# Kernel optimization log

Hardware: AMD Instinct MI355X
Metric: run time of the kernel (lower is better)

## Reference

```python
import jax, jax.numpy as jnp
import numpy as np

N_NODES = 100000
HIDDEN = 128
N_CLASS = 10
N_EDGES = 1600000


def setup_inputs() -> dict:
    key = jax.random.key(0)
    ks = jax.random.split(key, 8)
    s = 1.0 / np.sqrt(HIDDEN)
    return {
        "edge_index": jax.random.randint(ks[0], (2, N_EDGES), 0, N_NODES, dtype=jnp.int32),
        "embedding": jax.random.normal(ks[1], (N_NODES, HIDDEN), jnp.float32),
        "W1": jax.random.normal(ks[2], (HIDDEN, HIDDEN), jnp.float32) * s,
        "b1": jnp.zeros((HIDDEN,), jnp.float32),
        "W2": jax.random.normal(ks[3], (HIDDEN, HIDDEN), jnp.float32) * s,
        "b2": jnp.zeros((HIDDEN,), jnp.float32),
        "W_out": jax.random.normal(ks[4], (HIDDEN, N_CLASS), jnp.float32) * s,
        "b_out": jnp.zeros((N_CLASS,), jnp.float32),
    }


def reference(edge_index, embedding, W1, b1, W2, b2, W_out, b_out):
    N = embedding.shape[0]
    # PyG GCNConv: add self-loops, symmetric normalization D^-1/2 (A+I) D^-1/2
    loops = jnp.arange(N, dtype=edge_index.dtype)
    src = jnp.concatenate([edge_index[0], loops])  # message sources
    dst = jnp.concatenate([edge_index[1], loops])  # aggregation targets
    deg = jax.ops.segment_sum(jnp.ones_like(dst, jnp.float32), dst, num_segments=N)
    inv_sqrt = jnp.where(deg > 0, jax.lax.rsqrt(jnp.maximum(deg, 1.0)), 0.0)
    norm = inv_sqrt[src] * inv_sqrt[dst]  # [E+N]

    x = embedding  # forward ignores input x, uses learned embedding table
    for W, b in ((W1, b1), (W2, b2)):
        h = x @ W                                      # [N, H]
        msg = h[src] * norm[:, None]                   # gather + scale, [E+N, H]
        agg = jax.ops.segment_sum(msg, dst, num_segments=N)
        x = jax.nn.relu(agg + b)
    return x @ W_out + b_out
```

## Files before the change

kernel.cpp:

```cpp
#include <hip/hip_runtime.h>
#include <hip/hip_bf16.h>

#define HID 128
#define NCLASS 10
#define PCHUNK 8192
#define HB 256

typedef unsigned int uint;
typedef unsigned short ushort;
typedef __attribute__((ext_vector_type(8))) __bf16 bf16x8;
typedef __attribute__((ext_vector_type(4))) float f32x4;

__device__ __forceinline__ uint bf16rne(float x) {
    uint u = __float_as_uint(x);
    return (u + 0x7FFFu + ((u >> 16) & 1u)) >> 16;
}
__device__ __forceinline__ uint pack2(float e0, float e1) {
    return bf16rne(e0) | (bf16rne(e1) << 16);
}
__device__ __forceinline__ void unpack2(uint w, float& lo, float& hi) {
    lo = __uint_as_float(w << 16);
    hi = __uint_as_float(w & 0xFFFF0000u);
}
__device__ __forceinline__ void split2(float e0, float e1, uint& h, uint& l) {
    uint h0 = bf16rne(e0), h1 = bf16rne(e1);
    float r0 = e0 - __uint_as_float(h0 << 16);
    float r1 = e1 - __uint_as_float(h1 << 16);
    h = h0 | (h1 << 16);
    l = bf16rne(r0) | (bf16rne(r1) << 16);
}
__device__ __forceinline__ bf16x8 as_bf16x8(uint4 u) {
    return __builtin_bit_cast(bf16x8, u);
}
__device__ __forceinline__ void unpack8(uint4 u, float* f) {
    unpack2(u.x, f[0], f[1]); unpack2(u.y, f[2], f[3]);
    unpack2(u.z, f[4], f[5]); unpack2(u.w, f[6], f[7]);
}

__device__ __forceinline__ void pack_w_body(const float* __restrict__ W,
                                            uint* __restrict__ hi, uint* __restrict__ lo,
                                            int slot, int l) {
    const int s = slot >> 3, t = slot & 7;
    const int kb = s * 32 + (l >> 4) * 8, n = t * 16 + (l & 15);
    float f[8];
#pragma unroll
    for (int j = 0; j < 8; ++j) f[j] = W[(kb + j) * HID + n];
    uint4 h, lo4;
    split2(f[0], f[1], h.x, lo4.x);
    split2(f[2], f[3], h.y, lo4.y);
    split2(f[4], f[5], h.z, lo4.z);
    split2(f[6], f[7], h.w, lo4.w);
    const int fo = (slot * 64 + l) * 4;
    *(uint4*)(hi + fo) = h;
    *(uint4*)(lo + fo) = lo4;
}

__global__ __launch_bounds__(256) void hist_pack_kernel(
        const int* __restrict__ dst, int* __restrict__ bcnt, int E, int NB,
        const float* __restrict__ W1, uint* __restrict__ W1hi, uint* __restrict__ W1lo,
        const float* __restrict__ W2, uint* __restrict__ W2hi, uint* __restrict__ W2lo) {
    __shared__ int h[400];
    const int t = threadIdx.x;
    if ((int)blockIdx.x < HB) {
        const int ech = (E + HB - 1) / HB;
        const int e0 = blockIdx.x * ech;
        const int e1 = min(E, e0 + ech);
        for (int i = t; i < NB; i += 256) h[i] = 0;
        __syncthreads();
        for (int e = e0 + t; e < e1; e += 256) atomicAdd(&h[dst[e] >> 8], 1);
        __syncthreads();
        for (int i = t; i < NB; i += 256)
            if (h[i]) atomicAdd(&bcnt[i], h[i]);
    } else {
        const int pb = blockIdx.x - HB;
        const int slot = (pb & 7) * 4 + (t >> 6);
        const int l = t & 63;
        if (pb < 8) pack_w_body(W1, W1hi, W1lo, slot, l);
        else        pack_w_body(W2, W2hi, W2lo, slot, l);
    }
}

template <bool FP32IN>
__device__ __forceinline__ void gemm_body_mfma(
        const float* __restrict__ Xf, const uint* __restrict__ Xhi,
        const uint* __restrict__ Wphi, const uint* __restrict__ Wplo,
        ushort* __restrict__ HS, int N, int bidx, int tid) {
    const int wv = tid >> 6;
    const int l = tid & 63;
    const int q = l >> 4;
    const int cm = l & 15;
    const long rowbase = (long)bidx * 128 + wv * 32;

    bf16x8 bhi[2][4], blo[2][4];
#pragma unroll
    for (int rt = 0; rt < 2; ++rt) {
        const long row = rowbase + rt * 16 + cm;
        const long rc = row < N ? row : (N - 1);
#pragma unroll
        for (int s = 0; s < 4; ++s) {
            if (FP32IN) {
                const float* xp = Xf + rc * HID + s * 32 + q * 8;
                const float4 a0 = ((const float4*)xp)[0];
                const float4 a1 = ((const float4*)xp)[1];
                uint4 h, lo4;
                split2(a0.x, a0.y, h.x, lo4.x);
                split2(a0.z, a0.w, h.y, lo4.y);
                split2(a1.x, a1.y, h.z, lo4.z);
                split2(a1.z, a1.w, h.w, lo4.w);
                bhi[rt][s] = as_bf16x8(h);
                blo[rt][s] = as_bf16x8(lo4);
            } else {
                const long o = rc * (HID / 2) + s * 16 + q * 4;
                bhi[rt][s] = as_bf16x8(*(const uint4*)(Xhi + o));
            }
        }
    }

    f32x4 acc[2][8];
#pragma unroll
    for (int rt = 0; rt < 2; ++rt)
#pragma unroll
        for (int t = 0; t < 8; ++t) acc[rt][t] = (f32x4)0.0f;

#pragma unroll
    for (int s = 0; s < 4; ++s) {
#pragma unroll
        for (int t = 0; t < 8; ++t) {
            const int fo = ((s * 8 + t) * 64 + l) * 4;
            const bf16x8 whi = as_bf16x8(*(const uint4*)(Wphi + fo));
            const bf16x8 wlo = as_bf16x8(*(const uint4*)(Wplo + fo));
#pragma unroll
            for (int rt = 0; rt < 2; ++rt) {
                acc[rt][t] = __builtin_amdgcn_mfma_f32_16x16x32_bf16(whi, bhi[rt][s], acc[rt][t], 0, 0, 0);
                if (FP32IN)
                    acc[rt][t] = __builtin_amdgcn_mfma_f32_16x16x32_bf16(whi, blo[rt][s], acc[rt][t], 0, 0, 0);
                acc[rt][t] = __builtin_amdgcn_mfma_f32_16x16x32_bf16(wlo, bhi[rt][s], acc[rt][t], 0, 0, 0);
            }
        }
    }

#pragma unroll
    for (int rt = 0; rt < 2; ++rt) {
        const long row = rowbase + rt * 16 + cm;
        if (row < N) {
#pragma unroll
            for (int t = 0; t < 8; ++t) {
                uint2 o;
                o.x = pack2(acc[rt][t][0], acc[rt][t][1]);
                o.y = pack2(acc[rt][t][2], acc[rt][t][3]);
                *(uint2*)&HS[row * HID + t * 16 + q * 4] = o;
            }
        }
    }
}

__global__ __launch_bounds__(256) void gemm1_part_kernel(
        const float* __restrict__ emb, const uint* __restrict__ Wphi,
        const uint* __restrict__ Wplo, ushort* __restrict__ HS, int N,
        const int* __restrict__ src, const int* __restrict__ dst,
        int* __restrict__ gcursor, uint* __restrict__ staged, int E, int PB, int NB) {
    __shared__ int hist[400], lbase[400], loff[400];
    const int t = threadIdx.x;
    if ((int)blockIdx.x >= PB) {
        gemm_body_mfma<true>(emb, nullptr, Wphi, Wplo, HS, N, blockIdx.x - PB, t);
        return;
    }
    const int e0 = blockIdx.x * PCHUNK;
    for (int i = t; i < NB; i += 256) { hist[i] = 0; loff[i] = 0; }
    __syncthreads();
#pragma unroll
    for (int j = 0; j < PCHUNK / 256; ++j) {
        const int e = e0 + j * 256 + t;
        if (e < E) atomicAdd(&hist[dst[e] >> 8], 1);
    }
    __syncthreads();
    for (int b = t; b < NB; b += 256)
        if (hist[b] > 0) lbase[b] = atomicAdd(&gcursor[b], hist[b]);
    __syncthreads();
#pragma unroll
    for (int j = 0; j < PCHUNK / 256; ++j) {
        const int e = e0 + j * 256 + t;
        if (e < E) {
            const int d = dst[e];
            const int b = d >> 8;
            const int pos = lbase[b] + atomicAdd(&loff[b], 1);
            staged[pos] = (uint)src[e] | ((uint)(d & 255) << 17);
        }
    }
}

__global__ __launch_bounds__(256) void gemm2_kernel(
        const uint* __restrict__ Xhi, const uint* __restrict__ Wphi,
        const uint* __restrict__ Wplo, ushort* __restrict__ HS, int N) {
    gemm_body_mfma<false>(nullptr, Xhi, Wphi, Wplo, HS, N, blockIdx.x, threadIdx.x);
}

__global__ __launch_bounds__(512) void scan_buckets_kernel(const int* __restrict__ bcnt,
                                                           int* bbase, int* gcursor,
                                                           int* rps, int NB, int E, int N) {
    __shared__ int sh[512];
    const int t = threadIdx.x;
    const int v = (t < NB) ? bcnt[t] : 0;
    sh[t] = v;
    __syncthreads();
    for (int off = 1; off < 512; off <<= 1) {
        int x = (t >= off) ? sh[t - off] : 0;
        __syncthreads();
        sh[t] += x;
        __syncthreads();
    }
    const int excl = sh[t] - v;
    if (t < NB) { bbase[t] = excl; gcursor[t] = excl; }
    if (t == NB - 1) bbase[NB] = excl + v;
    if (t == 0) rps[N] = E;
}

__global__ __launch_bounds__(256) void fill_bucket_kernel(
        const uint* __restrict__ staged, const int* __restrict__ bbase,
        int* __restrict__ rps, float* __restrict__ invs, int* __restrict__ col, int N) {
    __shared__ int h[256], cur[256], sh[256];
    const int b = blockIdx.x, t = threadIdx.x;
    const int w0 = bbase[b], w1 = bbase[b + 1];
    const int base0 = b << 8;
    h[t] = 0;
    __syncthreads();
    for (int i = w0 + t; i < w1; i += 256) atomicAdd(&h[staged[i] >> 17], 1);
    __syncthreads();
    const int my = h[t];
    sh[t] = my;
    __syncthreads();
    for (int off = 1; off < 256; off <<= 1) {
        int x = (t >= off) ? sh[t - off] : 0;
        __syncthreads();
        sh[t] += x;
        __syncthreads();
    }
    const int start = w0 + sh[t] - my;
    cur[t] = start;
    const int node = base0 + t;
    if (node < N) {
        rps[node] = start;
        invs[node] = rsqrtf((float)my + 1.0f);
    }
    __syncthreads();
    for (int i = w0 + t; i < w1; i += 256) {
        const uint u = staged[i];
        const int p = atomicAdd(&cur[u >> 17], 1);
        col[p] = (int)(u & 0x1FFFFu);
    }
}

__global__ __launch_bounds__(256) void pull_relu_kernel(
        const int* __restrict__ rps, const int* __restrict__ col,
        const uint* __restrict__ HS, const float* __restrict__ invs,
        const float* __restrict__ b, uint* __restrict__ Xhi, int N) {
    const int g = blockIdx.x * 256 + threadIdx.x;
    const int node = g >> 3;
    if (node >= N) return;
    const int lane = g & 7;
    const int p = rps[node];
    const int d = rps[node + 1] - p;
    const uint4* H4 = (const uint4*)HS;
    const size_t so = (size_t)node * 16 + lane * 2;

    float acc[16];
    {
        const float sn = invs[node];
        float f[16];
        unpack8(H4[so], f);
        unpack8(H4[so + 1], f + 8);
#pragma unroll
        for (int j = 0; j < 16; ++j) acc[j] = f[j] * sn;
    }
    int i = 0;
    for (; i + 4 <= d; i += 4) {
        const int s0 = col[p + i], s1 = col[p + i + 1], s2 = col[p + i + 2], s3 = col[p + i + 3];
        const float w0 = invs[s0], w1 = invs[s1], w2 = invs[s2], w3 = invs[s3];
        const uint4 a0 = H4[(size_t)s0 * 16 + lane * 2], a0b = H4[(size_t)s0 * 16 + lane * 2 + 1];
        const uint4 a1 = H4[(size_t)s1 * 16 + lane * 2], a1b = H4[(size_t)s1 * 16 + lane * 2 + 1];
        const uint4 a2 = H4[(size_t)s2 * 16 + lane * 2], a2b = H4[(size_t)s2 * 16 + lane * 2 + 1];
        const uint4 a3 = H4[(size_t)s3 * 16 + lane * 2], a3b = H4[(size_t)s3 * 16 + lane * 2 + 1];
        float f[16];
        unpack8(a0, f); unpack8(a0b, f + 8);
#pragma unroll
        for (int j = 0; j < 16; ++j) acc[j] += f[j] * w0;
        unpack8(a1, f); unpack8(a1b, f + 8);
#pragma unroll
        for (int j = 0; j < 16; ++j) acc[j] += f[j] * w1;
        unpack8(a2, f); unpack8(a2b, f + 8);
#pragma unroll
        for (int j = 0; j < 16; ++j) acc[j] += f[j] * w2;
        unpack8(a3, f); unpack8(a3b, f + 8);
#pragma unroll
        for (int j = 0; j < 16; ++j) acc[j] += f[j] * w3;
    }
    for (; i < d; ++i) {
        const int s0 = col[p + i];
        const float w0 = invs[s0];
        const uint4 a0 = H4[(size_t)s0 * 16 + lane * 2], a0b = H4[(size_t)s0 * 16 + lane * 2 + 1];
        float f[16];
        unpack8(a0, f); unpack8(a0b, f + 8);
#pragma unroll
        for (int j = 0; j < 16; ++j) acc[j] += f[j] * w0;
    }
    const float sn = invs[node];
    float x[16];
#pragma unroll
    for (int j = 0; j < 16; ++j)
        x[j] = sn * fmaxf(acc[j] * sn + b[lane * 16 + j], 0.0f);
    uint4 h0, h1;
    h0.x = pack2(x[0], x[1]);   h0.y = pack2(x[2], x[3]);
    h0.z = pack2(x[4], x[5]);   h0.w = pack2(x[6], x[7]);
    h1.x = pack2(x[8], x[9]);   h1.y = pack2(x[10], x[11]);
    h1.z = pack2(x[12], x[13]); h1.w = pack2(x[14], x[15]);
    uint* oh = Xhi + (size_t)node * 64 + lane * 8;
    *(uint4*)oh = h0; *(uint4*)(oh + 4) = h1;
}

__global__ __launch_bounds__(256) void pull_out_kernel(
        const int* __restrict__ rps, const int* __restrict__ col,
        const uint* __restrict__ HS, const float* __restrict__ invs,
        const float* __restrict__ b2, const float* __restrict__ Wout,
        const float* __restrict__ bout, float* __restrict__ OUT, int N) {
    __shared__ float Wd[320 * 4];
    for (int t = threadIdx.x; t < 320; t += 256) {
        const int c = t >> 5, rem = t & 31, j4 = rem >> 3, l = rem & 7;
        const int k0 = l * 16 + j4 * 4;
        float4 w;
        w.x = Wout[(k0 + 0) * NCLASS + c];
        w.y = Wout[(k0 + 1) * NCLASS + c];
        w.z = Wout[(k0 + 2) * NCLASS + c];
        w.w = Wout[(k0 + 3) * NCLASS + c];
        ((float4*)Wd)[t] = w;
    }
    __syncthreads();

    const int g = blockIdx.x * 256 + threadIdx.x;
    const int node = g >> 3;
    if (node >= N) return;
    const int lane = g & 7;
    const int p = rps[node];
    const int d = rps[node + 1] - p;
    const uint4* H4 = (const uint4*)HS;
    const size_t so = (size_t)node * 16 + lane * 2;

    float acc[16];
    {
        float f[16];
        unpack8(H4[so], f);
        unpack8(H4[so + 1], f + 8);
#pragma unroll
        for (int j = 0; j < 16; ++j) acc[j] = f[j];
    }
    int i = 0;
    for (; i + 4 <= d; i += 4) {
        const int s0 = col[p + i], s1 = col[p + i + 1], s2 = col[p + i + 2], s3 = col[p + i + 3];
        const uint4 a0 = H4[(size_t)s0 * 16 + lane * 2], a0b = H4[(size_t)s0 * 16 + lane * 2 + 1];
        const uint4 a1 = H4[(size_t)s1 * 16 + lane * 2], a1b = H4[(size_t)s1 * 16 + lane * 2 + 1];
        const uint4 a2 = H4[(size_t)s2 * 16 + lane * 2], a2b = H4[(size_t)s2 * 16 + lane * 2 + 1];
        const uint4 a3 = H4[(size_t)s3 * 16 + lane * 2], a3b = H4[(size_t)s3 * 16 + lane * 2 + 1];
        float f[16];
        unpack8(a0, f); unpack8(a0b, f + 8);
#pragma unroll
        for (int j = 0; j < 16; ++j) acc[j] += f[j];
        unpack8(a1, f); unpack8(a1b, f + 8);
#pragma unroll
        for (int j = 0; j < 16; ++j) acc[j] += f[j];
        unpack8(a2, f); unpack8(a2b, f + 8);
#pragma unroll
        for (int j = 0; j < 16; ++j) acc[j] += f[j];
        unpack8(a3, f); unpack8(a3b, f + 8);
#pragma unroll
        for (int j = 0; j < 16; ++j) acc[j] += f[j];
    }
    for (; i < d; ++i) {
        const int s0 = col[p + i];
        const uint4 a0 = H4[(size_t)s0 * 16 + lane * 2], a0b = H4[(size_t)s0 * 16 + lane * 2 + 1];
        float f[16];
        unpack8(a0, f); unpack8(a0b, f + 8);
#pragma unroll
        for (int j = 0; j < 16; ++j) acc[j] += f[j];
    }
    const float sn = invs[node];
    float x[16];
#pragma unroll
    for (int j = 0; j < 16; ++j) x[j] = fmaxf(acc[j] * sn + b2[lane * 16 + j], 0.0f);

    const float4 xv0 = make_float4(x[0], x[1], x[2], x[3]);
    const float4 xv1 = make_float4(x[4], x[5], x[6], x[7]);
    const float4 xv2 = make_float4(x[8], x[9], x[10], x[11]);
    const float4 xv3 = make_float4(x[12], x[13], x[14], x[15]);
    const float4* Wd4 = (const float4*)Wd;
#pragma unroll
    for (int c = 0; c < NCLASS; ++c) {
        const float4* wp = Wd4 + c * 32 + lane;
        const float4 w0 = wp[0], w1 = wp[8], w2 = wp[16], w3 = wp[24];
        float s = xv0.x * w0.x + xv0.y * w0.y + xv0.z * w0.z + xv0.w * w0.w
                + xv1.x * w1.x + xv1.y * w1.y + xv1.z * w1.z + xv1.w * w1.w
                + xv2.x * w2.x + xv2.y * w2.y + xv2.z * w2.z + xv2.w * w2.w
                + xv3.x * w3.x + xv3.y * w3.y + xv3.z * w3.z + xv3.w * w3.w;
        s += __shfl_xor(s, 1, 8);
        s += __shfl_xor(s, 2, 8);
        s += __shfl_xor(s, 4, 8);
        if (lane == (c & 7)) OUT[(size_t)node * NCLASS + c] = s + bout[c];
    }
}

extern "C" void kernel_launch(void* const* d_in, const int* in_sizes, int n_in,
                              void* d_out, int out_size, void* d_ws, size_t ws_size,
                              hipStream_t stream) {
    const int* ei     = (const int*)d_in[0];
    const float* emb  = (const float*)d_in[1];
    const float* W1   = (const float*)d_in[2];
    const float* b1   = (const float*)d_in[3];
    const float* W2   = (const float*)d_in[4];
    const float* b2   = (const float*)d_in[5];
    const float* Wout = (const float*)d_in[6];
    const float* bout = (const float*)d_in[7];
    float* out        = (float*)d_out;

    const int E = in_sizes[0] / 2;
    const int N = in_sizes[1] / HID;
    const int* src = ei;
    const int* dst = ei + E;
    (void)ws_size; (void)n_in; (void)out_size;

    const int GB = (N + 127) / 128;
    const int NB = (N + 255) >> 8;
    const int PB = (E + PCHUNK - 1) / PCHUNK;

    char* ws = (char*)d_ws;
    size_t off = 0;
    auto alloc = [&](size_t bytes) {
        void* p = ws + off;
        off = (off + bytes + 4095) & ~(size_t)4095;
        return p;
    };
    int*   bcnt    = (int*)alloc(512 * 4);
    int*   bbase   = (int*)alloc(512 * 4);
    int*   gcursor = (int*)alloc(512 * 4);
    int*   rps     = (int*)alloc((size_t)(N + 1) * 4);
    float* invs    = (float*)alloc((size_t)N * 4);
    int*   col     = (int*)alloc((size_t)E * 4);
    uint*  staged  = (uint*)alloc((size_t)E * 4);
    uint*  Wp1hi   = (uint*)alloc(HID * HID * 2);
    uint*  Wp1lo   = (uint*)alloc(HID * HID * 2);
    uint*  Wp2hi   = (uint*)alloc(HID * HID * 2);
    uint*  Wp2lo   = (uint*)alloc(HID * HID * 2);
    uint*  HS      = (uint*)alloc((size_t)N * HID * 2);
    uint*  X1hi    = (uint*)alloc((size_t)N * HID * 2);

    hipMemsetAsync(bcnt, 0, 512 * 4, stream);
    hist_pack_kernel<<<HB + 16, 256, 0, stream>>>(dst, bcnt, E, NB,
                                                  W1, Wp1hi, Wp1lo, W2, Wp2hi, Wp2lo);
    scan_buckets_kernel<<<1, 512, 0, stream>>>(bcnt, bbase, gcursor, rps, NB, E, N);
    gemm1_part_kernel<<<PB + GB, 256, 0, stream>>>(emb, Wp1hi, Wp1lo, (ushort*)HS, N,
                                                   src, dst, gcursor, staged, E, PB, NB);
    fill_bucket_kernel<<<NB, 256, 0, stream>>>(staged, bbase, rps, invs, col, N);

    pull_relu_kernel<<<(N * 8 + 255) / 256, 256, 0, stream>>>(
        rps, col, HS, invs, b1, X1hi, N);

    gemm2_kernel<<<GB, 256, 0, stream>>>(X1hi, Wp2hi, Wp2lo, (ushort*)HS, N);
    pull_out_kernel<<<(N * 8 + 255) / 256, 256, 0, stream>>>(
        rps, col, HS, invs, b2, Wout, bout, out, N);
}
```

Before: 337.0 us.

## Fuse layer-1 aggregation with layer-2 GEMM through shared memory

Merges the layer-1 pull/ReLU kernel and the layer-2 MFMA GEMM into one kernel. Each block aggregates 32 nodes, stages the bf16 result in padded LDS, then multiplies it by W2 in place. This removes the intermediate X1 global write and read plus one launch. The price is an LDS barrier and smaller GEMM tiles that reload W2 fragments per 32-row block. The output kernel also coalesces its logit stores into one store per lane plus a tail.

```diff
diff --git a/kernel.cpp b/kernel.cpp
--- a/kernel.cpp
+++ b/kernel.cpp
@@ -80,11 +80,9 @@
     }
 }
 
-template <bool FP32IN>
-__device__ __forceinline__ void gemm_body_mfma(
-        const float* __restrict__ Xf, const uint* __restrict__ Xhi,
-        const uint* __restrict__ Wphi, const uint* __restrict__ Wplo,
-        ushort* __restrict__ HS, int N, int bidx, int tid) {
+__device__ __forceinline__ void gemm1_body(
+        const float* __restrict__ Xf, const uint* __restrict__ Wphi,
+        const uint* __restrict__ Wplo, ushort* __restrict__ HS, int N, int bidx, int tid) {
     const int wv = tid >> 6;
     const int l = tid & 63;
     const int q = l >> 4;
@@ -98,21 +96,16 @@
         const long rc = row < N ? row : (N - 1);
 #pragma unroll
         for (int s = 0; s < 4; ++s) {
-            if (FP32IN) {
-                const float* xp = Xf + rc * HID + s * 32 + q * 8;
-                const float4 a0 = ((const float4*)xp)[0];
-                const float4 a1 = ((const float4*)xp)[1];
-                uint4 h, lo4;
-                split2(a0.x, a0.y, h.x, lo4.x);
-                split2(a0.z, a0.w, h.y, lo4.y);
-                split2(a1.x, a1.y, h.z, lo4.z);
-                split2(a1.z, a1.w, h.w, lo4.w);
-                bhi[rt][s] = as_bf16x8(h);
-                blo[rt][s] = as_bf16x8(lo4);
-            } else {
-                const long o = rc * (HID / 2) + s * 16 + q * 4;
-                bhi[rt][s] = as_bf16x8(*(const uint4*)(Xhi + o));
-            }
+            const float* xp = Xf + rc * HID + s * 32 + q * 8;
+            const float4 a0 = ((const float4*)xp)[0];
+            const float4 a1 = ((const float4*)xp)[1];
+            uint4 h, lo4;
+            split2(a0.x, a0.y, h.x, lo4.x);
+            split2(a0.z, a0.w, h.y, lo4.y);
+            split2(a1.x, a1.y, h.z, lo4.z);
+            split2(a1.z, a1.w, h.w, lo4.w);
+            bhi[rt][s] = as_bf16x8(h);
+            blo[rt][s] = as_bf16x8(lo4);
         }
     }
 
@@ -132,8 +125,7 @@
 #pragma unroll
             for (int rt = 0; rt < 2; ++rt) {
                 acc[rt][t] = __builtin_amdgcn_mfma_f32_16x16x32_bf16(whi, bhi[rt][s], acc[rt][t], 0, 0, 0);
-                if (FP32IN)
-                    acc[rt][t] = __builtin_amdgcn_mfma_f32_16x16x32_bf16(whi, blo[rt][s], acc[rt][t], 0, 0, 0);
+                acc[rt][t] = __builtin_amdgcn_mfma_f32_16x16x32_bf16(whi, blo[rt][s], acc[rt][t], 0, 0, 0);
                 acc[rt][t] = __builtin_amdgcn_mfma_f32_16x16x32_bf16(wlo, bhi[rt][s], acc[rt][t], 0, 0, 0);
             }
         }
@@ -162,7 +154,7 @@
     __shared__ int hist[400], lbase[400], loff[400];
     const int t = threadIdx.x;
     if ((int)blockIdx.x >= PB) {
-        gemm_body_mfma<true>(emb, nullptr, Wphi, Wplo, HS, N, blockIdx.x - PB, t);
+        gemm1_body(emb, Wphi, Wplo, HS, N, blockIdx.x - PB, t);
         return;
     }
     const int e0 = blockIdx.x * PCHUNK;
@@ -187,12 +179,6 @@
             staged[pos] = (uint)src[e] | ((uint)(d & 255) << 17);
         }
     }
-}
-
-__global__ __launch_bounds__(256) void gemm2_kernel(
-        const uint* __restrict__ Xhi, const uint* __restrict__ Wphi,
-        const uint* __restrict__ Wplo, ushort* __restrict__ HS, int N) {
-    gemm_body_mfma<false>(nullptr, Xhi, Wphi, Wplo, HS, N, blockIdx.x, threadIdx.x);
 }
 
 __global__ __launch_bounds__(512) void scan_buckets_kernel(const int* __restrict__ bcnt,
@@ -250,76 +236,128 @@
     }
 }
 
-__global__ __launch_bounds__(256) void pull_relu_kernel(
+__global__ __launch_bounds__(256) void fused_mid_kernel(
         const int* __restrict__ rps, const int* __restrict__ col,
         const uint* __restrict__ HS, const float* __restrict__ invs,
-        const float* __restrict__ b, uint* __restrict__ Xhi, int N) {
-    const int g = blockIdx.x * 256 + threadIdx.x;
-    const int node = g >> 3;
-    if (node >= N) return;
-    const int lane = g & 7;
-    const int p = rps[node];
-    const int d = rps[node + 1] - p;
-    const uint4* H4 = (const uint4*)HS;
-    const size_t so = (size_t)node * 16 + lane * 2;
-
-    float acc[16];
+        const float* __restrict__ b1, const uint* __restrict__ Wphi,
+        const uint* __restrict__ Wplo, ushort* __restrict__ HS2, int N) {
+    __shared__ uint Xl[32 * 68];
+    uint4* Xl4 = (uint4*)Xl;
+    const int t = threadIdx.x;
+    const int base = blockIdx.x * 32;
+
     {
-        const float sn = invs[node];
-        float f[16];
-        unpack8(H4[so], f);
-        unpack8(H4[so + 1], f + 8);
-#pragma unroll
-        for (int j = 0; j < 16; ++j) acc[j] = f[j] * sn;
-    }
-    int i = 0;
-    for (; i + 4 <= d; i += 4) {
-        const int s0 = col[p + i], s1 = col[p + i + 1], s2 = col[p + i + 2], s3 = col[p + i + 3];
-        const float w0 = invs[s0], w1 = invs[s1], w2 = invs[s2], w3 = invs[s3];
-        const uint4 a0 = H4[(size_t)s0 * 16 + lane * 2], a0b = H4[(size_t)s0 * 16 + lane * 2 + 1];
-        const uint4 a1 = H4[(size_t)s1 * 16 + lane * 2], a1b = H4[(size_t)s1 * 16 + lane * 2 + 1];
-        const uint4 a2 = H4[(size_t)s2 * 16 + lane * 2], a2b = H4[(size_t)s2 * 16 + lane * 2 + 1];
-        const uint4 a3 = H4[(size_t)s3 * 16 + lane * 2], a3b = H4[(size_t)s3 * 16 + lane * 2 + 1];
-        float f[16];
-        unpack8(a0, f); unpack8(a0b, f + 8);
-#pragma unroll
-        for (int j = 0; j < 16; ++j) acc[j] += f[j] * w0;
-        unpack8(a1, f); unpack8(a1b, f + 8);
-#pragma unroll
-        for (int j = 0; j < 16; ++j) acc[j] += f[j] * w1;
-        unpack8(a2, f); unpack8(a2b, f + 8);
-#pragma unroll
-        for (int j = 0; j < 16; ++j) acc[j] += f[j] * w2;
-        unpack8(a3, f); unpack8(a3b, f + 8);
-#pragma unroll
-        for (int j = 0; j < 16; ++j) acc[j] += f[j] * w3;
-    }
-    for (; i < d; ++i) {
-        const int s0 = col[p + i];
-        const float w0 = invs[s0];
-        const uint4 a0 = H4[(size_t)s0 * 16 + lane * 2], a0b = H4[(size_t)s0 * 16 + lane * 2 + 1];
-        float f[16];
-        unpack8(a0, f); unpack8(a0b, f + 8);
-#pragma unroll
-        for (int j = 0; j < 16; ++j) acc[j] += f[j] * w0;
-    }
-    const float sn = invs[node];
-    float x[16];
-#pragma unroll
-    for (int j = 0; j < 16; ++j)
-        x[j] = sn * fmaxf(acc[j] * sn + b[lane * 16 + j], 0.0f);
-    uint4 h0, h1;
-    h0.x = pack2(x[0], x[1]);   h0.y = pack2(x[2], x[3]);
-    h0.z = pack2(x[4], x[5]);   h0.w = pack2(x[6], x[7]);
-    h1.x = pack2(x[8], x[9]);   h1.y = pack2(x[10], x[11]);
-    h1.z = pack2(x[12], x[13]); h1.w = pack2(x[14], x[15]);
-    uint* oh = Xhi + (size_t)node * 64 + lane * 8;
-    *(uint4*)oh = h0; *(uint4*)(oh + 4) = h1;
+        const int nl = t >> 3;
+        const int node = base + nl;
+        const int lane = t & 7;
+        uint4 h0 = make_uint4(0, 0, 0, 0), h1 = make_uint4(0, 0, 0, 0);
+        if (node < N) {
+            const int p = rps[node];
+            const int d = rps[node + 1] - p;
+            const float sn = invs[node];
+            const uint4* H4 = (const uint4*)HS;
+            const size_t so = (size_t)node * 16 + lane * 2;
+
+            float acc[16];
+            {
+                float f[16];
+                unpack8(H4[so], f);
+                unpack8(H4[so + 1], f + 8);
+#pragma unroll
+                for (int j = 0; j < 16; ++j) acc[j] = f[j] * sn;
+            }
+            int i = 0;
+            for (; i + 4 <= d; i += 4) {
+                const int s0 = col[p + i], s1 = col[p + i + 1];
+                const int s2 = col[p + i + 2], s3 = col[p + i + 3];
+                const float w0 = invs[s0], w1 = invs[s1], w2 = invs[s2], w3 = invs[s3];
+                const uint4 a0 = H4[(size_t)s0 * 16 + lane * 2], a0b = H4[(size_t)s0 * 16 + lane * 2 + 1];
+                const uint4 a1 = H4[(size_t)s1 * 16 + lane * 2], a1b = H4[(size_t)s1 * 16 + lane * 2 + 1];
+                const uint4 a2 = H4[(size_t)s2 * 16 + lane * 2], a2b = H4[(size_t)s2 * 16 + lane * 2 + 1];
+                const uint4 a3 = H4[(size_t)s3 * 16 + lane * 2], a3b = H4[(size_t)s3 * 16 + lane * 2 + 1];
+                float f[16];
+                unpack8(a0, f); unpack8(a0b, f + 8);
+#pragma unroll
+                for (int j = 0; j < 16; ++j) acc[j] += f[j] * w0;
+                unpack8(a1, f); unpack8(a1b, f + 8);
+#pragma unroll
+                for (int j = 0; j < 16; ++j) acc[j] += f[j] * w1;
+                unpack8(a2, f); unpack8(a2b, f + 8);
+#pragma unroll
+                for (int j = 0; j < 16; ++j) acc[j] += f[j] * w2;
+                unpack8(a3, f); unpack8(a3b, f + 8);
+#pragma unroll
+                for (int j = 0; j < 16; ++j) acc[j] += f[j] * w3;
+            }
+            for (; i < d; ++i) {
+                const int s0 = col[p + i];
+                const float w0 = invs[s0];
+                const uint4 a0 = H4[(size_t)s0 * 16 + lane * 2], a0b = H4[(size_t)s0 * 16 + lane * 2 + 1];
+                float f[16];
+                unpack8(a0, f); unpack8(a0b, f + 8);
+#pragma unroll
+                for (int j = 0; j < 16; ++j) acc[j] += f[j] * w0;
+            }
+            float x[16];
+#pragma unroll
+            for (int j = 0; j < 16; ++j)
+                x[j] = sn * fmaxf(acc[j] * sn + b1[lane * 16 + j], 0.0f);
+            h0.x = pack2(x[0], x[1]);   h0.y = pack2(x[2], x[3]);
+            h0.z = pack2(x[4], x[5]);   h0.w = pack2(x[6], x[7]);
+            h1.x = pack2(x[8], x[9]);   h1.y = pack2(x[10], x[11]);
+            h1.z = pack2(x[12], x[13]); h1.w = pack2(x[14], x[15]);
+        }
+        Xl4[nl * 17 + lane * 2]     = h0;
+        Xl4[nl * 17 + lane * 2 + 1] = h1;
+    }
+    __syncthreads();
+
+    {
+        const int wv = t >> 6;
+        const int l = t & 63;
+        const int q = l >> 4;
+        const int cm = l & 15;
+        const int rH = wv & 1;
+        const int cH = wv >> 1;
+        const int rl = rH * 16 + cm;
+
+        bf16x8 bh[4];
+#pragma unroll
+        for (int s = 0; s < 4; ++s) bh[s] = as_bf16x8(Xl4[rl * 17 + s * 4 + q]);
+
+        f32x4 acc[4];
+#pragma unroll
+        for (int tt = 0; tt < 4; ++tt) acc[tt] = (f32x4)0.0f;
+
+#pragma unroll
+        for (int s = 0; s < 4; ++s) {
+#pragma unroll
+            for (int tt = 0; tt < 4; ++tt) {
+                const int tg = cH * 4 + tt;
+                const int fo = ((s * 8 + tg) * 64 + l) * 4;
+                const bf16x8 whi = as_bf16x8(*(const uint4*)(Wphi + fo));
+                const bf16x8 wlo = as_bf16x8(*(const uint4*)(Wplo + fo));
+                acc[tt] = __builtin_amdgcn_mfma_f32_16x16x32_bf16(whi, bh[s], acc[tt], 0, 0, 0);
+                acc[tt] = __builtin_amdgcn_mfma_f32_16x16x32_bf16(wlo, bh[s], acc[tt], 0, 0, 0);
+            }
+        }
+
+        const long row = (long)base + rl;
+        if (row < N) {
+#pragma unroll
+            for (int tt = 0; tt < 4; ++tt) {
+                uint2 o;
+                o.x = pack2(acc[tt][0], acc[tt][1]);
+                o.y = pack2(acc[tt][2], acc[tt][3]);
+                *(uint2*)&HS2[row * HID + cH * 64 + tt * 16 + q * 4] = o;
+            }
+        }
+    }
 }
 
 __global__ __launch_bounds__(256) void pull_out_kernel(
         const int* __restrict__ rps, const int* __restrict__ col,
-        const uint* __restrict__ HS, const float* __restrict__ invs,
+        const uint* __restrict__ HS2, const float* __restrict__ invs,
         const float* __restrict__ b2, const float* __restrict__ Wout,
         const float* __restrict__ bout, float* __restrict__ OUT, int N) {
     __shared__ float Wd[320 * 4];
@@ -341,7 +379,7 @@
     const int lane = g & 7;
     const int p = rps[node];
     const int d = rps[node + 1] - p;
-    const uint4* H4 = (const uint4*)HS;
+    const uint4* H4 = (const uint4*)HS2;
     const size_t so = (size_t)node * 16 + lane * 2;
 
     float acc[16];
@@ -391,6 +429,7 @@
     const float4 xv2 = make_float4(x[8], x[9], x[10], x[11]);
     const float4 xv3 = make_float4(x[12], x[13], x[14], x[15]);
     const float4* Wd4 = (const float4*)Wd;
+    float resA = 0.0f, resB = 0.0f;
 #pragma unroll
     for (int c = 0; c < NCLASS; ++c) {
         const float4* wp = Wd4 + c * 32 + lane;
@@ -402,8 +441,11 @@
         s += __shfl_xor(s, 1, 8);
         s += __shfl_xor(s, 2, 8);
         s += __shfl_xor(s, 4, 8);
-        if (lane == (c & 7)) OUT[(size_t)node * NCLASS + c] = s + bout[c];
-    }
+        if (c < 8) { if (lane == c) resA = s; }
+        else       { if (lane == c - 8) resB = s; }
+    }
+    OUT[(size_t)node * NCLASS + lane] = resA + bout[lane];
+    if (lane < 2) OUT[(size_t)node * NCLASS + 8 + lane] = resB + bout[8 + lane];
 }
 
 extern "C" void kernel_launch(void* const* d_in, const int* in_sizes, int n_in,
@@ -426,6 +468,7 @@
     (void)ws_size; (void)n_in; (void)out_size;
 
     const int GB = (N + 127) / 128;
+    const int FB = (N + 31) / 32;
     const int NB = (N + 255) >> 8;
     const int PB = (E + PCHUNK - 1) / PCHUNK;
 
@@ -448,7 +491,7 @@
     uint*  Wp2hi   = (uint*)alloc(HID * HID * 2);
     uint*  Wp2lo   = (uint*)alloc(HID * HID * 2);
     uint*  HS      = (uint*)alloc((size_t)N * HID * 2);
-    uint*  X1hi    = (uint*)alloc((size_t)N * HID * 2);
+    uint*  HS2     = (uint*)alloc((size_t)N * HID * 2);
 
     hipMemsetAsync(bcnt, 0, 512 * 4, stream);
     hist_pack_kernel<<<HB + 16, 256, 0, stream>>>(dst, bcnt, E, NB,
@@ -458,10 +501,8 @@
                                                    src, dst, gcursor, staged, E, PB, NB);
     fill_bucket_kernel<<<NB, 256, 0, stream>>>(staged, bbase, rps, invs, col, N);
 
-    pull_relu_kernel<<<(N * 8 + 255) / 256, 256, 0, stream>>>(
-        rps, col, HS, invs, b1, X1hi, N);
-
-    gemm2_kernel<<<GB, 256, 0, stream>>>(X1hi, Wp2hi, Wp2lo, (ushort*)HS, N);
-    pull_out_kernel<<<(N * 8 + 255) / 256, 256, 0, stream>>>(
-        rps, col, HS, invs, b2, Wout, bout, out, N);
-}
+    fused_mid_kernel<<<FB, 256, 0, stream>>>(rps, col, HS, invs, b1,
+                                             Wp2hi, Wp2lo, (ushort*)HS2, N);
+
+    pull_out_kernel<<<FB, 256, 0, stream>>>(rps, col, HS2, invs, b2, Wout, bout, out, N);
+}
```

Result: faster. 317.6 us (-5.8%).
